# Performance work log

Hardware: AMD Instinct MI355X
Metric: run time of the kernel (lower is better)

## Reference

```python
import jax, jax.numpy as jnp
import numpy as np

B, C, HW, SCALE = 8, 512, 64, 8
M = C // SCALE  # Q/K channel dim
EPS = 1e-6


def setup_inputs() -> dict:
    key = jax.random.key(0)
    ks = jax.random.split(key, 8)
    s = 0.02
    return {
        "x": jax.random.normal(ks[0], (B, C, HW, HW), dtype=jnp.float32),
        "wq": jax.random.normal(ks[1], (M, C), dtype=jnp.float32) * s,
        "bq": jax.random.normal(ks[2], (M,), dtype=jnp.float32) * s,
        "wk": jax.random.normal(ks[3], (M, C), dtype=jnp.float32) * s,
        "bk": jax.random.normal(ks[4], (M,), dtype=jnp.float32) * s,
        "wv": jax.random.normal(ks[5], (C, C), dtype=jnp.float32) * s,
        "bv": jax.random.normal(ks[6], (C,), dtype=jnp.float32) * s,
        "gamma": jax.random.normal(ks[7], (1,), dtype=jnp.float32),
    }


def reference(x, wq, bq, wk, bk, wv, bv, gamma):
    b, c, w, h = x.shape
    n = w * h
    xf = x.reshape(b, c, n)  # [B,C,N]
    # 1x1 convs == channel GEMMs
    Q = jnp.einsum('bcn,mc->bmn', xf, wq) + bq[None, :, None]  # [B,M,N]
    K = jnp.einsum('bcn,mc->bmn', xf, wk) + bk[None, :, None]  # [B,M,N]
    V = jnp.einsum('bcn,oc->bon', xf, wv) + bv[None, :, None]  # [B,C,N]
    # pooling gate: global max + global avg over spatial dims -> [B,C,1]
    gate = (jnp.max(xf, axis=-1) + jnp.mean(xf, axis=-1))[:, :, None]
    V = gate * V
    Qf = jax.nn.softplus(Q).transpose(0, 2, 1)  # [B,N,M]
    Kf = jax.nn.softplus(K)                      # [B,M,N]
    KV = jnp.einsum('bmn,bcn->bmc', Kf, V)       # [B,M,C]
    norm = 1.0 / jnp.einsum('bnm,bm->bn', Qf, jnp.sum(Kf, axis=-1) + EPS)  # [B,N]
    wval = jnp.einsum('bnm,bmc,bn->bcn', Qf, KV, norm)  # [B,C,N]
    wval = wval.reshape(b, c, h, w)
    return x + gamma * wval
```

## Files before the change

### kernel.cpp

```cpp
#include <hip/hip_runtime.h>
#include <math.h>

#define Bb 8
#define Cc 512
#define Nn 4096
#define Mm 64
#define OC 640
#define EPSf 1e-6f

typedef unsigned short ushort_t;
typedef unsigned int uint_t;
typedef __attribute__((ext_vector_type(8))) short short8;
typedef __attribute__((ext_vector_type(4))) float f32x4;

constexpr size_t OFF_GATE = 0;
constexpr size_t OFF_BCAT = OFF_GATE + (size_t)Bb * Cc;
constexpr size_t OFF_GPM  = OFF_BCAT + (size_t)OC;
constexpr size_t OFF_GPS  = OFF_GPM + (size_t)64 * Bb * Cc;
constexpr size_t OFF_WBF  = OFF_GPS + (size_t)64 * Bb * Cc;
constexpr size_t OFF_XT   = OFF_WBF + (size_t)OC * Cc / 2;
constexpr size_t OFF_QBF  = OFF_XT + (size_t)Bb * Nn * Cc / 2;
constexpr size_t OFF_KBF  = OFF_QBF + (size_t)Bb * Mm * Nn / 2;
constexpr size_t OFF_VBF  = OFF_KBF + (size_t)Bb * Mm * Nn / 2;
constexpr size_t OFF_KVBF = OFF_VBF + (size_t)Bb * Cc * Nn / 2;
constexpr size_t OFF_KSUM = OFF_KVBF + (size_t)Bb * Cc * Mm / 2;
constexpr size_t OFF_NORM = OFF_KSUM + (size_t)Bb * Mm;
constexpr size_t OFF_QT   = OFF_NORM + (size_t)Bb * Nn;

__device__ __forceinline__ float softplus_f(float v) {
    return fmaxf(v, 0.f) + __logf(1.f + __expf(-fabsf(v)));
}
__device__ __forceinline__ ushort_t f2bf(float f) {
    uint_t u = __float_as_uint(f);
    uint_t r = (u + 0x7fffu + ((u >> 16) & 1u)) >> 16;
    return (ushort_t)r;
}
__device__ __forceinline__ float bf2f(ushort_t h) {
    return __uint_as_float(((uint_t)h) << 16);
}
__device__ __forceinline__ void gload_lds16(const void* g, void* l) {
    __builtin_amdgcn_global_load_lds(
        (const __attribute__((address_space(1))) unsigned int*)g,
        (__attribute__((address_space(3))) unsigned int*)l, 16, 0, 0);
}
#define BARRIER()   asm volatile("s_barrier" ::: "memory")
#define WAIT_VM(N)  asm volatile("s_waitcnt vmcnt(" #N ")" ::: "memory")

__global__ void wconv_k(const float* __restrict__ wq, const float* __restrict__ bq,
                        const float* __restrict__ wk, const float* __restrict__ bk,
                        const float* __restrict__ wv, const float* __restrict__ bv,
                        ushort_t* __restrict__ wbf, float* __restrict__ bcat) {
    int i = blockIdx.x * 256 + threadIdx.x;
    if (i < OC * Cc) {
        int o = i / Cc, c = i % Cc;
        float v;
        if (o < Mm)            v = wq[o * Cc + c];
        else if (o < 2 * Mm)   v = wk[(o - Mm) * Cc + c];
        else                   v = wv[(o - 2 * Mm) * Cc + c];
        wbf[i] = f2bf(v);
    }
    if (i < OC) {
        float v;
        if (i < Mm)            v = bq[i];
        else if (i < 2 * Mm)   v = bk[i - Mm];
        else                   v = bv[i - 2 * Mm];
        bcat[i] = v;
    }
}

__global__ __launch_bounds__(256) void xtrans_k(const float* __restrict__ x, ushort_t* __restrict__ xT,
                                                float* __restrict__ gpm, float* __restrict__ gps) {
    const int nb = blockIdx.x * 64;
    const int cb = blockIdx.y * 64;
    const int b  = blockIdx.z;
    __shared__ float Xt[64][65];
    __shared__ float pmx[4][64], psm[4][64];
    const int t = threadIdx.x;
    #pragma unroll
    for (int it = 0; it < 4; it++) {
        int cl = it * 16 + (t >> 4);
        int n0 = (t & 15) * 4;
        float4 v = *(const float4*)(x + ((size_t)b * Cc + cb + cl) * Nn + nb + n0);
        Xt[cl][n0 + 0] = v.x;
        Xt[cl][n0 + 1] = v.y;
        Xt[cl][n0 + 2] = v.z;
        Xt[cl][n0 + 3] = v.w;
    }
    __syncthreads();
    #pragma unroll
    for (int r = 0; r < 8; r++) {
        int nl = (t >> 5) + r * 8;
        int c0 = (t & 31) * 2;
        uint_t pk = (uint_t)f2bf(Xt[c0][nl]) | ((uint_t)f2bf(Xt[c0 + 1][nl]) << 16);
        *(uint_t*)(xT + ((size_t)b * Nn + nb + nl) * Cc + cb + c0) = pk;
    }
    {
        int cl = t & 63, q = t >> 6;
        float mx = -3.4e38f, sm = 0.f;
        #pragma unroll
        for (int j = 0; j < 16; j++) {
            float v = Xt[cl][q * 16 + j];
            mx = fmaxf(mx, v); sm += v;
        }
        pmx[q][cl] = mx; psm[q][cl] = sm;
    }
    __syncthreads();
    if (t < 64) {
        float mx = fmaxf(fmaxf(pmx[0][t], pmx[1][t]), fmaxf(pmx[2][t], pmx[3][t]));
        float sm = psm[0][t] + psm[1][t] + psm[2][t] + psm[3][t];
        size_t idx = (size_t)blockIdx.x * (Bb * Cc) + (size_t)b * Cc + cb + t;
        gpm[idx] = mx;
        gps[idx] = sm;
    }
}

__global__ void gatered_k(const float* __restrict__ gpm, const float* __restrict__ gps,
                          float* __restrict__ gate) {
    int bc = blockIdx.x;
    int l = threadIdx.x;
    float mx = gpm[(size_t)l * (Bb * Cc) + bc];
    float sm = gps[(size_t)l * (Bb * Cc) + bc];
    #pragma unroll
    for (int off = 32; off; off >>= 1) {
        mx = fmaxf(mx, __shfl_xor(mx, off));
        sm += __shfl_xor(sm, off);
    }
    if (l == 0) gate[bc] = mx + sm * (1.f / Nn);
}

__global__ __launch_bounds__(256, 4) void qkv_mfma_k(const ushort_t* __restrict__ wbf,
                                                     const ushort_t* __restrict__ xT,
                                                     const float* __restrict__ bcat,
                                                     ushort_t* __restrict__ Qbf,
                                                     ushort_t* __restrict__ Kbf,
                                                     ushort_t* __restrict__ Vbf,
                                                     float* __restrict__ Ksum) {
    const int nb  = blockIdx.x * 128;
    const int oty = blockIdx.y;
    const int b   = blockIdx.z;
    __shared__ ushort_t At[3][2048];
    __shared__ ushort_t Bt[3][4096];
    const int tid  = threadIdx.x;
    const int w    = tid >> 6;
    const int lane = tid & 63;
    const int wr   = w >> 1, wc = w & 1;
    const int hi   = lane >> 4, lo = lane & 15;
    const int rA   = tid >> 2;
    const int kc   = (((tid & 3) ^ ((tid >> 3) & 3)) * 8);
    const int sx   = (hi ^ ((lo >> 1) & 3)) * 8;
    const ushort_t* xb = xT + ((size_t)b * Nn + nb) * Cc;
    const ushort_t* wb = wbf + (size_t)oty * 64 * Cc;

    f32x4 acc[2][4] = {};

    auto stage = [&](int buf, int kb) {
        gload_lds16(wb + (size_t)rA * Cc + kb + kc,        &At[buf][w * 512]);
        gload_lds16(xb + (size_t)rA * Cc + kb + kc,        &Bt[buf][w * 512]);
        gload_lds16(xb + (size_t)(64 + rA) * Cc + kb + kc, &Bt[buf][2048 + w * 512]);
    };
    auto compute = [&](int buf) {
        short8 a[2], bfr[4];
        #pragma unroll
        for (int mi = 0; mi < 2; mi++)
            a[mi] = *(const short8*)(&At[buf][(wr * 32 + mi * 16 + lo) * 32 + sx]);
        #pragma unroll
        for (int ni = 0; ni < 4; ni++)
            bfr[ni] = *(const short8*)(&Bt[buf][(wc * 64 + ni * 16 + lo) * 32 + sx]);
        #pragma unroll
        for (int mi = 0; mi < 2; mi++)
            #pragma unroll
            for (int ni = 0; ni < 4; ni++)
                acc[mi][ni] = __builtin_amdgcn_mfma_f32_16x16x32_bf16(a[mi], bfr[ni], acc[mi][ni], 0, 0, 0);
    };

    stage(0, 0);
    stage(1, 32);
    #pragma unroll
    for (int t = 0; t < 16; ++t) {
        if (t < 15) { WAIT_VM(3); } else { WAIT_VM(0); }
        BARRIER();
        if (t + 2 < 16) stage((t + 2) % 3, (t + 2) * 32);
        compute(t % 3);
    }

    if (oty == 0) {
        #pragma unroll
        for (int mi = 0; mi < 2; mi++)
            #pragma unroll
            for (int r = 0; r < 4; r++) {
                const int ol = wr * 32 + mi * 16 + hi * 4 + r;
                const float bias = bcat[ol];
                ushort_t* dst = Qbf + ((size_t)b * Mm + ol) * Nn + nb + wc * 64;
                #pragma unroll
                for (int ni = 0; ni < 4; ni++)
                    dst[ni * 16 + lo] = f2bf(softplus_f(acc[mi][ni][r] + bias));
            }
    } else if (oty == 1) {
        #pragma unroll
        for (int mi = 0; mi < 2; mi++)
            #pragma unroll
            for (int r = 0; r < 4; r++) {
                const int ol = wr * 32 + mi * 16 + hi * 4 + r;
                const float bias = bcat[Mm + ol];
                ushort_t* dst = Kbf + ((size_t)b * Mm + ol) * Nn + nb + wc * 64;
                float s = 0.f;
                #pragma unroll
                for (int ni = 0; ni < 4; ni++) {
                    float sp = softplus_f(acc[mi][ni][r] + bias);
                    dst[ni * 16 + lo] = f2bf(sp);
                    s += sp;
                }
                s += __shfl_xor(s, 1); s += __shfl_xor(s, 2);
                s += __shfl_xor(s, 4); s += __shfl_xor(s, 8);
                if (lo == 0) atomicAdd(&Ksum[b * Mm + ol], s);
            }
    } else {
        const int cbase = (oty - 2) * 64;
        #pragma unroll
        for (int mi = 0; mi < 2; mi++)
            #pragma unroll
            for (int r = 0; r < 4; r++) {
                const int ol = wr * 32 + mi * 16 + hi * 4 + r;
                const float bias = bcat[oty * 64 + ol];
                ushort_t* dst = Vbf + ((size_t)b * Cc + cbase + ol) * Nn + nb + wc * 64;
                #pragma unroll
                for (int ni = 0; ni < 4; ni++)
                    dst[ni * 16 + lo] = f2bf(acc[mi][ni][r] + bias);
            }
    }
}

__global__ __launch_bounds__(256, 4) void kv_mfma_k(const ushort_t* __restrict__ Kbf,
                                                    const ushort_t* __restrict__ Vbf,
                                                    float* __restrict__ KVpart) {
    const int cb = blockIdx.x * 128;
    const int split = blockIdx.y;
    const int b = blockIdx.z;
    __shared__ ushort_t Vt[3][4096];
    __shared__ ushort_t Kt[3][2048];
    const int tid = threadIdx.x;
    const int w = tid >> 6, lane = tid & 63;
    const int hi = lane >> 4, lo = lane & 15;
    const int rwl = lane >> 2;
    const int kc  = (((lane & 3) ^ ((lane >> 3) & 3)) * 8);
    const int sx  = (hi ^ ((lo >> 1) & 3)) * 8;
    const ushort_t* Vb = Vbf + (size_t)b * Cc * Nn;
    const ushort_t* Kb = Kbf + (size_t)b * Mm * Nn;
    const int nbase = split * 512;

    f32x4 acc[2][4] = {};

    auto stage = [&](int buf, int n0) {
        #pragma unroll
        for (int li = 0; li < 2; li++) {
            const int rw = (w * 2 + li) * 16 + rwl;
            gload_lds16(Vb + (size_t)(cb + rw) * Nn + n0 + kc, &Vt[buf][(w * 2 + li) * 512]);
        }
        gload_lds16(Kb + (size_t)(w * 16 + rwl) * Nn + n0 + kc, &Kt[buf][w * 512]);
    };
    auto compute = [&](int buf) {
        short8 a[2], bv[4];
        #pragma unroll
        for (int mi = 0; mi < 2; mi++)
            a[mi] = *(const short8*)(&Vt[buf][(w * 32 + mi * 16 + lo) * 32 + sx]);
        #pragma unroll
        for (int ni = 0; ni < 4; ni++)
            bv[ni] = *(const short8*)(&Kt[buf][(ni * 16 + lo) * 32 + sx]);
        #pragma unroll
        for (int mi = 0; mi < 2; mi++)
            #pragma unroll
            for (int ni = 0; ni < 4; ni++)
                acc[mi][ni] = __builtin_amdgcn_mfma_f32_16x16x32_bf16(a[mi], bv[ni], acc[mi][ni], 0, 0, 0);
    };

    stage(0, nbase);
    stage(1, nbase + 32);
    #pragma unroll
    for (int t = 0; t < 16; ++t) {
        if (t < 15) { WAIT_VM(3); } else { WAIT_VM(0); }
        BARRIER();
        if (t + 2 < 16) stage((t + 2) % 3, nbase + (t + 2) * 32);
        compute(t % 3);
    }

    float* dst = KVpart + (size_t)(split * Bb + b) * Cc * Mm;
    #pragma unroll
    for (int mi = 0; mi < 2; mi++)
        #pragma unroll
        for (int r = 0; r < 4; r++) {
            const int c = cb + w * 32 + mi * 16 + hi * 4 + r;
            #pragma unroll
            for (int ni = 0; ni < 4; ni++)
                dst[(size_t)c * Mm + ni * 16 + lo] = acc[mi][ni][r];
        }
}

__global__ __launch_bounds__(256) void kvred_k(const float* __restrict__ KVpart,
                                               const float* __restrict__ gate,
                                               ushort_t* __restrict__ KVbf) {
    int i = blockIdx.x * 256 + threadIdx.x;
    const f32x4* p = (const f32x4*)KVpart;
    f32x4 s = p[i];
    #pragma unroll
    for (int sp = 1; sp < 8; sp++) s += p[(size_t)sp * 65536 + i];
    int idx4 = i * 4;
    int b = idx4 >> 15;
    int c = (idx4 >> 6) & (Cc - 1);
    float g = gate[b * Cc + c];
    uint2 pk;
    pk.x = (uint_t)f2bf(s[0] * g) | ((uint_t)f2bf(s[1] * g) << 16);
    pk.y = (uint_t)f2bf(s[2] * g) | ((uint_t)f2bf(s[3] * g) << 16);
    *(uint2*)(KVbf + (size_t)i * 4) = pk;
}

__global__ __launch_bounds__(256) void qtransnorm_k(const ushort_t* __restrict__ Qbf,
                                                    const float* __restrict__ Ksum,
                                                    ushort_t* __restrict__ QT,
                                                    float* __restrict__ normb) {
    const int n0 = blockIdx.x * 64;
    const int b  = blockIdx.y;
    __shared__ float Qs[64][65];
    __shared__ float ks[64];
    __shared__ float ps[4][64];
    const int t = threadIdx.x;
    if (t < 64) ks[t] = Ksum[b * Mm + t] + EPSf;
    {
        int m = t >> 2, q = t & 3;
        const ushort_t* src = Qbf + ((size_t)b * Mm + m) * Nn + n0 + q * 16;
        short8 v0 = *(const short8*)(src);
        short8 v1 = *(const short8*)(src + 8);
        #pragma unroll
        for (int j = 0; j < 8; j++) {
            Qs[m][q * 16 + j]     = bf2f((ushort_t)v0[j]);
            Qs[m][q * 16 + 8 + j] = bf2f((ushort_t)v1[j]);
        }
    }
    __syncthreads();
    {
        int n = t & 63, ch = t >> 6;
        float s = 0.f;
        #pragma unroll
        for (int j = 0; j < 16; j++) s += Qs[ch * 16 + j][n] * ks[ch * 16 + j];
        ps[ch][n] = s;
    }
    __syncthreads();
    if (t < 64) normb[(size_t)b * Nn + n0 + t] = 1.f / (ps[0][t] + ps[1][t] + ps[2][t] + ps[3][t]);
    #pragma unroll
    for (int i = 0; i < 2; i++) {
        int u = t + i * 256;
        int n = u >> 3, j = u & 7;
        short8 v;
        #pragma unroll
        for (int jj = 0; jj < 8; jj++) v[jj] = (short)f2bf(Qs[j * 8 + jj][n]);
        *(short8*)(QT + ((size_t)b * Nn + n0 + n) * Mm + j * 8) = v;
    }
}

__global__ __launch_bounds__(256, 4) void final_mfma_k(const float* __restrict__ x,
                                                       const ushort_t* __restrict__ QT,
                                                       const ushort_t* __restrict__ KVbf,
                                                       const float* __restrict__ normb,
                                                       const float* __restrict__ gamma,
                                                       float* __restrict__ out) {
    const int nb = blockIdx.x * 128;
    const int cb = blockIdx.y * 128;
    const int b  = blockIdx.z;
    __shared__ ushort_t Qs[128 * 64];
    __shared__ ushort_t Ks[128 * 64];
    const int tid  = threadIdx.x;
    const int w    = tid >> 6;
    const int lane = tid & 63;
    const int wr   = w >> 1, wc = w & 1;
    const int hi   = lane >> 4, lo = lane & 15;
    const int lr   = lane >> 3;
    const int swz  = (((lane & 7) ^ (lr & 7)) * 8);
    const ushort_t* Qb = QT + (size_t)b * Nn * Mm;
    const ushort_t* Kb = KVbf + (size_t)b * Cc * Mm;

    #pragma unroll
    for (int p = 0; p < 4; p++) {
        const int rb = p * 32 + w * 8;
        gload_lds16(Qb + (size_t)(nb + rb + lr) * Mm + swz, &Qs[rb * 64]);
        gload_lds16(Kb + (size_t)(cb + rb + lr) * Mm + swz, &Ks[rb * 64]);
    }
    __syncthreads();

    f32x4 acc[4][4] = {};
    #pragma unroll
    for (int kk = 0; kk < 2; kk++) {
        short8 a[4], bfr[4];
        #pragma unroll
        for (int mi = 0; mi < 4; mi++) {
            const int row = wr * 64 + mi * 16 + lo;
            a[mi] = *(const short8*)(&Qs[row * 64 + (((kk * 4 + hi) ^ (lo & 7)) * 8)]);
        }
        #pragma unroll
        for (int ni = 0; ni < 4; ni++) {
            const int row = wc * 64 + ni * 16 + lo;
            bfr[ni] = *(const short8*)(&Ks[row * 64 + (((kk * 4 + hi) ^ (lo & 7)) * 8)]);
        }
        #pragma unroll
        for (int mi = 0; mi < 4; mi++)
            #pragma unroll
            for (int ni = 0; ni < 4; ni++)
                acc[mi][ni] = __builtin_amdgcn_mfma_f32_16x16x32_bf16(a[mi], bfr[ni], acc[mi][ni], 0, 0, 0);
    }

    const float g = gamma[0];
    #pragma unroll
    for (int mi = 0; mi < 4; mi++) {
        const int n0 = nb + wr * 64 + mi * 16 + hi * 4;
        float4 nrm = *(const float4*)(normb + (size_t)b * Nn + n0);
        #pragma unroll
        for (int ni = 0; ni < 4; ni++) {
            const int c = cb + wc * 64 + ni * 16 + lo;
            size_t idx = ((size_t)b * Cc + c) * Nn + n0;
            float4 xv = *(const float4*)(x + idx);
            float4 o;
            o.x = xv.x + g * nrm.x * acc[mi][ni][0];
            o.y = xv.y + g * nrm.y * acc[mi][ni][1];
            o.z = xv.z + g * nrm.z * acc[mi][ni][2];
            o.w = xv.w + g * nrm.w * acc[mi][ni][3];
            *(float4*)(out + idx) = o;
        }
    }
}

extern "C" void kernel_launch(void* const* d_in, const int* in_sizes, int n_in,
                              void* d_out, int out_size, void* d_ws, size_t ws_size,
                              hipStream_t stream) {
    const float* x     = (const float*)d_in[0];
    const float* wq    = (const float*)d_in[1];
    const float* bq    = (const float*)d_in[2];
    const float* wk    = (const float*)d_in[3];
    const float* bk    = (const float*)d_in[4];
    const float* wv    = (const float*)d_in[5];
    const float* bv    = (const float*)d_in[6];
    const float* gamma = (const float*)d_in[7];
    float* out = (float*)d_out;
    float* ws  = (float*)d_ws;

    float*    gate   = ws + OFF_GATE;
    float*    bcat   = ws + OFF_BCAT;
    float*    gpm    = ws + OFF_GPM;
    float*    gps    = ws + OFF_GPS;
    ushort_t* wbf    = (ushort_t*)(ws + OFF_WBF);
    ushort_t* xT     = (ushort_t*)(ws + OFF_XT);
    float*    KVpart = ws + OFF_XT;
    ushort_t* Qbf    = (ushort_t*)(ws + OFF_QBF);
    ushort_t* Kbf    = (ushort_t*)(ws + OFF_KBF);
    ushort_t* Vbf    = (ushort_t*)(ws + OFF_VBF);
    ushort_t* KVbf   = (ushort_t*)(ws + OFF_KVBF);
    float*    Ksum   = ws + OFF_KSUM;
    float*    normb  = ws + OFF_NORM;
    ushort_t* QT     = (ushort_t*)(ws + OFF_QT);

    wconv_k<<<(OC * Cc + 255) / 256, 256, 0, stream>>>(wq, bq, wk, bk, wv, bv, wbf, bcat);
    xtrans_k<<<dim3(Nn / 64, Cc / 64, Bb), 256, 0, stream>>>(x, xT, gpm, gps);
    gatered_k<<<Bb * Cc, 64, 0, stream>>>(gpm, gps, gate);
    hipMemsetAsync(Ksum, 0, (size_t)Bb * Mm * sizeof(float), stream);
    qkv_mfma_k<<<dim3(Nn / 128, OC / 64, Bb), 256, 0, stream>>>(wbf, xT, bcat, Qbf, Kbf, Vbf, Ksum);
    kv_mfma_k<<<dim3(Cc / 128, 8, Bb), 256, 0, stream>>>(Kbf, Vbf, KVpart);
    kvred_k<<<(Bb * Cc * Mm / 4) / 256, 256, 0, stream>>>(KVpart, gate, KVbf);
    qtransnorm_k<<<dim3(Nn / 64, Bb), 256, 0, stream>>>(Qbf, Ksum, QT, normb);
    final_mfma_k<<<dim3(Nn / 128, Cc / 128, Bb), 256, 0, stream>>>(x, QT, KVbf, normb, gamma, out);
}
```

Before: 119.1 us.

## Write Q transposed from QKV GEMM and compute norm inside final kernel

The QKV GEMM epilogue now writes softplus(Q) directly in [N,M] layout, which removes the separate qtransnorm transpose kernel. The per-row normaliser is recomputed inside the final MFMA kernel from the Q tile already in LDS, and the result is kept in shared memory instead of a global buffer. The K row sums move from atomics in the GEMM epilogue to a separate ksum kernel that reads back the bf16 K, which also drops the memset. The trade-offs are redundant norm computation across the four channel blocks, an extra launch plus a read of K, and Ksum now summed from bf16-rounded values.

```diff
diff --git a/kernel.cpp b/kernel.cpp
--- a/kernel.cpp
+++ b/kernel.cpp
@@ -19,13 +19,11 @@
 constexpr size_t OFF_GPS  = OFF_GPM + (size_t)64 * Bb * Cc;
 constexpr size_t OFF_WBF  = OFF_GPS + (size_t)64 * Bb * Cc;
 constexpr size_t OFF_XT   = OFF_WBF + (size_t)OC * Cc / 2;
-constexpr size_t OFF_QBF  = OFF_XT + (size_t)Bb * Nn * Cc / 2;
-constexpr size_t OFF_KBF  = OFF_QBF + (size_t)Bb * Mm * Nn / 2;
+constexpr size_t OFF_QT   = OFF_XT + (size_t)Bb * Nn * Cc / 2;
+constexpr size_t OFF_KBF  = OFF_QT + (size_t)Bb * Mm * Nn / 2;
 constexpr size_t OFF_VBF  = OFF_KBF + (size_t)Bb * Mm * Nn / 2;
 constexpr size_t OFF_KVBF = OFF_VBF + (size_t)Bb * Cc * Nn / 2;
 constexpr size_t OFF_KSUM = OFF_KVBF + (size_t)Bb * Cc * Mm / 2;
-constexpr size_t OFF_NORM = OFF_KSUM + (size_t)Bb * Mm;
-constexpr size_t OFF_QT   = OFF_NORM + (size_t)Bb * Nn;
 
 __device__ __forceinline__ float softplus_f(float v) {
     return fmaxf(v, 0.f) + __logf(1.f + __expf(-fabsf(v)));
@@ -131,10 +129,9 @@
 __global__ __launch_bounds__(256, 4) void qkv_mfma_k(const ushort_t* __restrict__ wbf,
                                                      const ushort_t* __restrict__ xT,
                                                      const float* __restrict__ bcat,
-                                                     ushort_t* __restrict__ Qbf,
+                                                     ushort_t* __restrict__ QT,
                                                      ushort_t* __restrict__ Kbf,
-                                                     ushort_t* __restrict__ Vbf,
-                                                     float* __restrict__ Ksum) {
+                                                     ushort_t* __restrict__ Vbf) {
     const int nb  = blockIdx.x * 128;
     const int oty = blockIdx.y;
     const int b   = blockIdx.z;
@@ -184,17 +181,23 @@
     }
 
     if (oty == 0) {
-        #pragma unroll
-        for (int mi = 0; mi < 2; mi++)
-            #pragma unroll
-            for (int r = 0; r < 4; r++) {
-                const int ol = wr * 32 + mi * 16 + hi * 4 + r;
-                const float bias = bcat[ol];
-                ushort_t* dst = Qbf + ((size_t)b * Mm + ol) * Nn + nb + wc * 64;
-                #pragma unroll
-                for (int ni = 0; ni < 4; ni++)
-                    dst[ni * 16 + lo] = f2bf(softplus_f(acc[mi][ni][r] + bias));
+        ushort_t* qt = QT + ((size_t)b * Nn + nb + wc * 64) * Mm + wr * 32 + hi * 4;
+        #pragma unroll
+        for (int mi = 0; mi < 2; mi++) {
+            const int mb = wr * 32 + mi * 16 + hi * 4;
+            #pragma unroll
+            for (int ni = 0; ni < 4; ni++) {
+                const int n = ni * 16 + lo;
+                float s0 = softplus_f(acc[mi][ni][0] + bcat[mb + 0]);
+                float s1 = softplus_f(acc[mi][ni][1] + bcat[mb + 1]);
+                float s2 = softplus_f(acc[mi][ni][2] + bcat[mb + 2]);
+                float s3 = softplus_f(acc[mi][ni][3] + bcat[mb + 3]);
+                uint2 pk;
+                pk.x = (uint_t)f2bf(s0) | ((uint_t)f2bf(s1) << 16);
+                pk.y = (uint_t)f2bf(s2) | ((uint_t)f2bf(s3) << 16);
+                *(uint2*)(qt + (size_t)n * Mm + mi * 16) = pk;
             }
+        }
     } else if (oty == 1) {
         #pragma unroll
         for (int mi = 0; mi < 2; mi++)
@@ -203,16 +206,9 @@
                 const int ol = wr * 32 + mi * 16 + hi * 4 + r;
                 const float bias = bcat[Mm + ol];
                 ushort_t* dst = Kbf + ((size_t)b * Mm + ol) * Nn + nb + wc * 64;
-                float s = 0.f;
                 #pragma unroll
-                for (int ni = 0; ni < 4; ni++) {
-                    float sp = softplus_f(acc[mi][ni][r] + bias);
-                    dst[ni * 16 + lo] = f2bf(sp);
-                    s += sp;
-                }
-                s += __shfl_xor(s, 1); s += __shfl_xor(s, 2);
-                s += __shfl_xor(s, 4); s += __shfl_xor(s, 8);
-                if (lo == 0) atomicAdd(&Ksum[b * Mm + ol], s);
+                for (int ni = 0; ni < 4; ni++)
+                    dst[ni * 16 + lo] = f2bf(softplus_f(acc[mi][ni][r] + bias));
             }
     } else {
         const int cbase = (oty - 2) * 64;
@@ -228,6 +224,24 @@
                     dst[ni * 16 + lo] = f2bf(acc[mi][ni][r] + bias);
             }
     }
+}
+
+__global__ __launch_bounds__(256) void ksum_k(const ushort_t* __restrict__ Kbf, float* __restrict__ Ksum) {
+    int bm = blockIdx.x;
+    const ushort_t* row = Kbf + (size_t)bm * Nn;
+    int t = threadIdx.x;
+    float sm = 0.f;
+    for (int i = t * 8; i < Nn; i += 2048) {
+        short8 v = *(const short8*)(row + i);
+        #pragma unroll
+        for (int j = 0; j < 8; j++) sm += bf2f((ushort_t)v[j]);
+    }
+    #pragma unroll
+    for (int off = 32; off; off >>= 1) sm += __shfl_xor(sm, off);
+    __shared__ float ssm[4];
+    if ((t & 63) == 0) ssm[t >> 6] = sm;
+    __syncthreads();
+    if (t == 0) Ksum[bm] = ssm[0] + ssm[1] + ssm[2] + ssm[3];
 }
 
 __global__ __launch_bounds__(256, 4) void kv_mfma_k(const ushort_t* __restrict__ Kbf,
@@ -313,53 +327,10 @@
     *(uint2*)(KVbf + (size_t)i * 4) = pk;
 }
 
-__global__ __launch_bounds__(256) void qtransnorm_k(const ushort_t* __restrict__ Qbf,
-                                                    const float* __restrict__ Ksum,
-                                                    ushort_t* __restrict__ QT,
-                                                    float* __restrict__ normb) {
-    const int n0 = blockIdx.x * 64;
-    const int b  = blockIdx.y;
-    __shared__ float Qs[64][65];
-    __shared__ float ks[64];
-    __shared__ float ps[4][64];
-    const int t = threadIdx.x;
-    if (t < 64) ks[t] = Ksum[b * Mm + t] + EPSf;
-    {
-        int m = t >> 2, q = t & 3;
-        const ushort_t* src = Qbf + ((size_t)b * Mm + m) * Nn + n0 + q * 16;
-        short8 v0 = *(const short8*)(src);
-        short8 v1 = *(const short8*)(src + 8);
-        #pragma unroll
-        for (int j = 0; j < 8; j++) {
-            Qs[m][q * 16 + j]     = bf2f((ushort_t)v0[j]);
-            Qs[m][q * 16 + 8 + j] = bf2f((ushort_t)v1[j]);
-        }
-    }
-    __syncthreads();
-    {
-        int n = t & 63, ch = t >> 6;
-        float s = 0.f;
-        #pragma unroll
-        for (int j = 0; j < 16; j++) s += Qs[ch * 16 + j][n] * ks[ch * 16 + j];
-        ps[ch][n] = s;
-    }
-    __syncthreads();
-    if (t < 64) normb[(size_t)b * Nn + n0 + t] = 1.f / (ps[0][t] + ps[1][t] + ps[2][t] + ps[3][t]);
-    #pragma unroll
-    for (int i = 0; i < 2; i++) {
-        int u = t + i * 256;
-        int n = u >> 3, j = u & 7;
-        short8 v;
-        #pragma unroll
-        for (int jj = 0; jj < 8; jj++) v[jj] = (short)f2bf(Qs[j * 8 + jj][n]);
-        *(short8*)(QT + ((size_t)b * Nn + n0 + n) * Mm + j * 8) = v;
-    }
-}
-
 __global__ __launch_bounds__(256, 4) void final_mfma_k(const float* __restrict__ x,
                                                        const ushort_t* __restrict__ QT,
                                                        const ushort_t* __restrict__ KVbf,
-                                                       const float* __restrict__ normb,
+                                                       const float* __restrict__ Ksum,
                                                        const float* __restrict__ gamma,
                                                        float* __restrict__ out) {
     const int nb = blockIdx.x * 128;
@@ -367,6 +338,8 @@
     const int b  = blockIdx.z;
     __shared__ ushort_t Qs[128 * 64];
     __shared__ ushort_t Ks[128 * 64];
+    __shared__ float ksS[Mm];
+    __shared__ float nrmS[128];
     const int tid  = threadIdx.x;
     const int w    = tid >> 6;
     const int lane = tid & 63;
@@ -383,7 +356,20 @@
         gload_lds16(Qb + (size_t)(nb + rb + lr) * Mm + swz, &Qs[rb * 64]);
         gload_lds16(Kb + (size_t)(cb + rb + lr) * Mm + swz, &Ks[rb * 64]);
     }
+    if (tid < Mm) ksS[tid] = Ksum[b * Mm + tid] + EPSf;
     __syncthreads();
+
+    if (tid < 128) {
+        const int r = tid;
+        float sv = 0.f;
+        #pragma unroll
+        for (int s = 0; s < 8; s++) {
+            short8 v = *(const short8*)(&Qs[r * 64 + ((s ^ (r & 7)) * 8)]);
+            #pragma unroll
+            for (int e = 0; e < 8; e++) sv += bf2f((ushort_t)v[e]) * ksS[s * 8 + e];
+        }
+        nrmS[r] = 1.f / sv;
+    }
 
     f32x4 acc[4][4] = {};
     #pragma unroll
@@ -405,12 +391,14 @@
             for (int ni = 0; ni < 4; ni++)
                 acc[mi][ni] = __builtin_amdgcn_mfma_f32_16x16x32_bf16(a[mi], bfr[ni], acc[mi][ni], 0, 0, 0);
     }
+    __syncthreads();
 
     const float g = gamma[0];
     #pragma unroll
     for (int mi = 0; mi < 4; mi++) {
-        const int n0 = nb + wr * 64 + mi * 16 + hi * 4;
-        float4 nrm = *(const float4*)(normb + (size_t)b * Nn + n0);
+        const int rl = wr * 64 + mi * 16 + hi * 4;
+        const int n0 = nb + rl;
+        float4 nrm = *(const float4*)(&nrmS[rl]);
         #pragma unroll
         for (int ni = 0; ni < 4; ni++) {
             const int c = cb + wc * 64 + ni * 16 + lo;
@@ -447,21 +435,18 @@
     ushort_t* wbf    = (ushort_t*)(ws + OFF_WBF);
     ushort_t* xT     = (ushort_t*)(ws + OFF_XT);
     float*    KVpart = ws + OFF_XT;
-    ushort_t* Qbf    = (ushort_t*)(ws + OFF_QBF);
+    ushort_t* QT     = (ushort_t*)(ws + OFF_QT);
     ushort_t* Kbf    = (ushort_t*)(ws + OFF_KBF);
     ushort_t* Vbf    = (ushort_t*)(ws + OFF_VBF);
     ushort_t* KVbf   = (ushort_t*)(ws + OFF_KVBF);
     float*    Ksum   = ws + OFF_KSUM;
-    float*    normb  = ws + OFF_NORM;
-    ushort_t* QT     = (ushort_t*)(ws + OFF_QT);
 
     wconv_k<<<(OC * Cc + 255) / 256, 256, 0, stream>>>(wq, bq, wk, bk, wv, bv, wbf, bcat);
     xtrans_k<<<dim3(Nn / 64, Cc / 64, Bb), 256, 0, stream>>>(x, xT, gpm, gps);
     gatered_k<<<Bb * Cc, 64, 0, stream>>>(gpm, gps, gate);
-    hipMemsetAsync(Ksum, 0, (size_t)Bb * Mm * sizeof(float), stream);
-    qkv_mfma_k<<<dim3(Nn / 128, OC / 64, Bb), 256, 0, stream>>>(wbf, xT, bcat, Qbf, Kbf, Vbf, Ksum);
+    qkv_mfma_k<<<dim3(Nn / 128, OC / 64, Bb), 256, 0, stream>>>(wbf, xT, bcat, QT, Kbf, Vbf);
+    ksum_k<<<Bb * Mm, 256, 0, stream>>>(Kbf, Ksum);
     kv_mfma_k<<<dim3(Cc / 128, 8, Bb), 256, 0, stream>>>(Kbf, Vbf, KVpart);
     kvred_k<<<(Bb * Cc * Mm / 4) / 256, 256, 0, stream>>>(KVpart, gate, KVbf);
-    qtransnorm_k<<<dim3(Nn / 64, Bb), 256, 0, stream>>>(Qbf, Ksum, QT, normb);
-    final_mfma_k<<<dim3(Nn / 128, Cc / 128, Bb), 256, 0, stream>>>(x, QT, KVbf, normb, gamma, out);
-}
+    final_mfma_k<<<dim3(Nn / 128, Cc / 128, Bb), 256, 0, stream>>>(x, QT, KVbf, Ksum, gamma, out);
+}
```

Result: no change. 119.0 us (-0.1%).
